# Kernel optimization log

Hardware: AMD Instinct MI355X
Metric: run time of the kernel (lower is better)

## Reference

```python
import jax, jax.numpy as jnp
import numpy as np

NUM_FRAMES = 8
HEAD_DIM = 32


def setup_inputs() -> dict:
    key = jax.random.key(0)
    k1, k2, k3, k4, k5 = jax.random.split(key, 5)
    dim = 384
    nh = dim // HEAD_DIM
    return {
        "x": jax.random.normal(k1, (16, dim, 16, 16), dtype=jnp.float32),
        "qk_w": jax.random.normal(k2, (2 * dim, dim), dtype=jnp.float32) * 0.02,
        "alpha": jax.random.normal(k3, (1, nh, 1, 1), dtype=jnp.float32),
        "beta": jax.random.normal(k4, (1, nh, 1, 1), dtype=jnp.float32),
        "gamma": jax.random.normal(k5, (1, nh, 1, 1), dtype=jnp.float32),
    }


def reference(x, qk_w, alpha, beta, gamma):
    B_T, C, H, W = x.shape
    B = B_T // NUM_FRAMES
    N = NUM_FRAMES * H * W
    nh = C // HEAD_DIM
    scale = HEAD_DIM ** -0.5

    # [B*T,C,H,W] -> [B,N,C] tokens (frames-major token order, matching torch)
    xt = x.reshape(B, NUM_FRAMES, C, H, W).transpose(0, 2, 1, 3, 4)  # B,C,T,H,W
    xt = xt.reshape(B, C, N).transpose(0, 2, 1)                      # B,N,C

    qk = (xt @ qk_w.T).reshape(B, N, 2, nh, HEAD_DIM)
    qk = qk.transpose(2, 0, 3, 1, 4)                                 # 2,B,nh,N,hd
    q, k = qk[0], qk[1]
    v = xt.reshape(B, N, nh, HEAD_DIM).transpose(0, 2, 1, 3)         # B,nh,N,hd

    attn = jax.nn.softmax(jnp.einsum('bhnd,bhmd->bhnm', q * scale, k), axis=-1)
    eye = jnp.eye(N, dtype=x.dtype)
    Cm = jnp.full((N, N), 1.0 / N, dtype=x.dtype)
    attn = alpha * eye + beta * attn - gamma * Cm                    # B,nh,N,N

    out = jnp.einsum('bhnm,bhmd->bhnd', attn, v)
    out = out.transpose(0, 2, 1, 3).reshape(B, N, C)                 # B,N,C
    out = out.transpose(0, 2, 1).reshape(B, C, NUM_FRAMES, H, W)
    out = out.transpose(0, 2, 1, 3, 4).reshape(B_T, C, H, W)
    return out
```

## Files before the change

kernel.cpp:

```cpp
#include <hip/hip_runtime.h>
#include <hip/hip_bf16.h>

typedef __attribute__((ext_vector_type(8))) short short8;
typedef __attribute__((ext_vector_type(4))) float f32x4;
typedef __attribute__((ext_vector_type(16))) float f32x16;
typedef __attribute__((ext_vector_type(4))) unsigned int uint4v;
typedef unsigned short ushort_t;
typedef unsigned int uint_t;

#define NFRAMES 8
#define HD 32
#define CDIM 384
#define NH 12
#define NTOK 2048
#define QKCOLS 768
#define TILEB 2048
#define QSCALE 0.2550541213313367f

static __device__ __forceinline__ ushort_t f2bf(float f) {
    __hip_bfloat16 h = __float2bfloat16(f);
    return *reinterpret_cast<ushort_t*>(&h);
}
static __device__ __forceinline__ uint_t packbf2(float lo, float hi) {
    return (uint_t)f2bf(lo) | ((uint_t)f2bf(hi) << 16);
}

__global__ __launch_bounds__(256) void pack_x_kernel(const float* __restrict__ x,
                                                     ushort_t* __restrict__ Xt,
                                                     ushort_t* __restrict__ VFG,
                                                     float* __restrict__ psum) {
    __shared__ float lds[32 * 256];
    __shared__ float red[8][32];
    int bt = blockIdx.x;
    int h = blockIdx.y;
    int tid = threadIdx.x;
    int c0 = h * 32;
    const float* src = x + ((long)bt * CDIM + c0) * 256;
#pragma unroll
    for (int i = 0; i < 32; ++i) lds[i * 256 + tid] = src[i * 256 + tid];
    __syncthreads();
    int b = bt >> 3, t = bt & 7;
    long n = (long)b * NTOK + t * 256 + tid;
    uint4* dst = reinterpret_cast<uint4*>(Xt + n * CDIM + c0);
#pragma unroll
    for (int k = 0; k < 4; ++k) {
        uint_t vv[4];
#pragma unroll
        for (int q = 0; q < 4; ++q)
            vv[q] = packbf2(lds[(k * 8 + q * 2) * 256 + tid], lds[(k * 8 + q * 2 + 1) * 256 + tid]);
        dst[k] = make_uint4(vv[0], vv[1], vv[2], vv[3]);
    }
    int bh = b * NH + h;
#pragma unroll
    for (int pass = 0; pass < 4; ++pass) {
        int kt = pass * 2 + (tid >> 7);
        int slot = tid & 127;
        int d = slot & 31, c2 = slot >> 5;
        const float* p0 = &lds[d * 256 + kt * 32 + c2 * 8];
        float4 a = *(const float4*)p0;
        float4 bb = *(const float4*)(p0 + 4);
        uint4 o = make_uint4(packbf2(a.x, a.y), packbf2(a.z, a.w),
                             packbf2(bb.x, bb.y), packbf2(bb.z, bb.w));
        *(uint4*)((char*)VFG + ((size_t)(bh * 64 + t * 8 + kt)) * TILEB + slot * 16) = o;
    }
    int ch = tid & 31, seg = tid >> 5;
    float s = 0.f;
#pragma unroll
    for (int j = 0; j < 32; ++j) s += lds[ch * 256 + seg * 32 + j];
    red[seg][ch] = s;
    __syncthreads();
    if (tid < 32) {
        float tot = 0.f;
#pragma unroll
        for (int i = 0; i < 8; ++i) tot += red[i][tid];
        psum[(bt * NH + h) * HD + tid] = tot;
    }
}

__global__ __launch_bounds__(256) void pack_w_kernel(const float* __restrict__ w,
                                                     ushort_t* __restrict__ Wb) {
    int idx = blockIdx.x * 256 + threadIdx.x;
    if (idx >= QKCOLS * CDIM) return;
    int j = idx / CDIM;
    float scale = (j < CDIM) ? QSCALE : 1.0f;
    Wb[idx] = f2bf(w[idx] * scale);
}

__global__ __launch_bounds__(256) void proj_kernel(const ushort_t* __restrict__ Xt,
                                                   const ushort_t* __restrict__ Wb,
                                                   ushort_t* __restrict__ QFG,
                                                   ushort_t* __restrict__ KFG) {
    __shared__ __align__(16) ushort_t tb[4][32][40];
    int tid = threadIdx.x;
    int lane = tid & 63;
    int w = tid >> 6;
    int wid = blockIdx.x * 4 + w;
    int mb = wid / 24, nb = wid % 24;
    int r16 = lane & 15, g = lane >> 4;
    const short8* A0 = reinterpret_cast<const short8*>(Xt + (mb * 32 + r16) * CDIM + g * 8);
    const short8* A1 = reinterpret_cast<const short8*>(Xt + (mb * 32 + 16 + r16) * CDIM + g * 8);
    const short8* B0 = reinterpret_cast<const short8*>(Wb + (nb * 32 + r16) * CDIM + g * 8);
    const short8* B1 = reinterpret_cast<const short8*>(Wb + (nb * 32 + 16 + r16) * CDIM + g * 8);
    f32x4 acc00{}, acc01{}, acc10{}, acc11{};
#pragma unroll
    for (int kk = 0; kk < 12; ++kk) {
        short8 a0 = A0[kk * 4];
        short8 a1 = A1[kk * 4];
        short8 b0 = B0[kk * 4];
        short8 b1 = B1[kk * 4];
        acc00 = __builtin_amdgcn_mfma_f32_16x16x32_bf16(a0, b0, acc00, 0, 0, 0);
        acc01 = __builtin_amdgcn_mfma_f32_16x16x32_bf16(a0, b1, acc01, 0, 0, 0);
        acc10 = __builtin_amdgcn_mfma_f32_16x16x32_bf16(a1, b0, acc10, 0, 0, 0);
        acc11 = __builtin_amdgcn_mfma_f32_16x16x32_bf16(a1, b1, acc11, 0, 0, 0);
    }
#pragma unroll
    for (int r = 0; r < 4; ++r) {
        int lr = g * 4 + r;
        tb[w][lr][r16] = f2bf(acc00[r]);
        tb[w][lr][r16 + 16] = f2bf(acc01[r]);
        tb[w][lr + 16][r16] = f2bf(acc10[r]);
        tb[w][lr + 16][r16 + 16] = f2bf(acc11[r]);
    }
    short8 f0 = *(const short8*)&tb[w][lane & 31][(lane >> 5) * 8];
    short8 f1 = *(const short8*)&tb[w][lane & 31][16 + (lane >> 5) * 8];
    int bsel = mb >> 6;
    int tile = mb & 63;
    int hh = (nb < 12) ? nb : nb - 12;
    ushort_t* dstbuf = (nb < 12) ? QFG : KFG;
    char* base = (char*)dstbuf + ((size_t)((bsel * NH + hh) * 64 + tile)) * TILEB;
    *(short8*)(base + lane * 16) = f0;
    *(short8*)(base + 1024 + lane * 16) = f1;
}

__global__ __launch_bounds__(256) void attn_kernel(
    const ushort_t* __restrict__ QFG, const ushort_t* __restrict__ KFG,
    const ushort_t* __restrict__ VFG, const float* __restrict__ x,
    const float* __restrict__ psum, const float* __restrict__ alpha,
    const float* __restrict__ beta, const float* __restrict__ gamma,
    float* __restrict__ out) {
    __shared__ float mrg[2240];

    int tid = threadIdx.x, lane = tid & 63, w = tid >> 6;
    int bid = blockIdx.x;
    int L = (bid & 7) * 96 + (bid >> 3);
    int rb = L & 31, bh = L >> 5;
    int h = bh % NH, b = bh / NH;
    int j31 = lane & 31, hi = lane >> 5;
    int qsub = w >> 1, kvpar = w & 1;
    int qb = rb * 64 + qsub * 32;

    const char* Qb = (const char*)QFG + ((size_t)(bh * 64 + rb * 2 + qsub)) * TILEB;
    short8 qf0 = *(const short8*)(Qb + lane * 16);
    short8 qf1 = *(const short8*)(Qb + 1024 + lane * 16);

    const char* Kbase = (const char*)KFG + (size_t)bh * 64 * TILEB + lane * 16;
    const char* Vbase = (const char*)VFG + (size_t)bh * 64 * TILEB + lane * 16;

    f32x16 acc = {};
    float lp = 0.f;

    short8 kA0, kA1, vA0, vA1, kB0, kB1, vB0, vB1;

#define LOADT(i, K0, K1, V0, V1)                                         \
    {                                                                    \
        size_t off = (size_t)(2 * (i) + kvpar) * TILEB;                  \
        K0 = *(const short8*)(Kbase + off);                              \
        K1 = *(const short8*)(Kbase + off + 1024);                       \
        V0 = *(const short8*)(Vbase + off);                              \
        V1 = *(const short8*)(Vbase + off + 1024);                       \
    }

#define COMPUTE(K0, K1, V0, V1)                                          \
    {                                                                    \
        f32x16 s = {};                                                   \
        s = __builtin_amdgcn_mfma_f32_32x32x16_bf16(K0, qf0, s, 0, 0, 0);\
        s = __builtin_amdgcn_mfma_f32_32x32x16_bf16(K1, qf1, s, 0, 0, 0);\
        float e[16];                                                     \
        _Pragma("unroll")                                                \
        for (int r = 0; r < 16; ++r) e[r] = __builtin_amdgcn_exp2f(s[r]);\
        lp += (((e[0] + e[1]) + (e[2] + e[3])) + ((e[4] + e[5]) + (e[6] + e[7]))) +  \
              (((e[8] + e[9]) + (e[10] + e[11])) + ((e[12] + e[13]) + (e[14] + e[15]))); \
        uint_t pk[8];                                                    \
        _Pragma("unroll")                                                \
        for (int j = 0; j < 8; ++j) pk[j] = packbf2(e[2 * j], e[2 * j + 1]); \
        _Pragma("unroll")                                                \
        for (int kh = 0; kh < 2; ++kh) {                                 \
            uint_t o0 = pk[kh * 4], o1 = pk[kh * 4 + 1];                 \
            uint_t o2 = pk[kh * 4 + 2], o3 = pk[kh * 4 + 3];             \
            uint_t s0_ = hi ? o0 : o2, s1_ = hi ? o1 : o3;               \
            uint_t g0 = __shfl_xor(s0_, 32), g1 = __shfl_xor(s1_, 32);   \
            uint4v uu;                                                   \
            uu[0] = hi ? g0 : o0;                                        \
            uu[1] = hi ? g1 : o1;                                        \
            uu[2] = hi ? o2 : g0;                                        \
            uu[3] = hi ? o3 : g1;                                        \
            short8 pa = __builtin_bit_cast(short8, uu);                  \
            acc = __builtin_amdgcn_mfma_f32_32x32x16_bf16(pa, (kh ? V1 : V0), acc, 0, 0, 0); \
        }                                                                \
    }

    LOADT(0, kA0, kA1, vA0, vA1);
#pragma unroll 2
    for (int i2 = 0; i2 < 16; ++i2) {
        int i = i2 * 2;
        if (i + 1 < 32) LOADT(i + 1, kB0, kB1, vB0, vB1);
        COMPUTE(kA0, kA1, vA0, vA1);
        if (i + 2 < 32) LOADT(i + 2, kA0, kA1, vA0, vA1);
        COMPUTE(kB0, kB1, vB0, vB1);
    }
#undef LOADT
#undef COMPUTE

    float* ab = mrg + qsub * 1088;
    if (kvpar) {
#pragma unroll
        for (int q = 0; q < 16; ++q) ab[lane * 17 + q] = acc[q];
        ab[lane * 17 + 16] = lp;
    }
    __syncthreads();
    float* Lb = mrg + 2176 + qsub * 32;
    if (!kvpar) {
#pragma unroll
        for (int q = 0; q < 16; ++q) acc[q] += ab[lane * 17 + q];
        float lsum = lp + ab[lane * 17 + 16];
        lsum += __shfl_xor(lsum, 32);
        if (!hi) Lb[j31] = lsum;
    }
    __syncthreads();
    if (!kvpar) {
        float alpha_h = alpha[h], beta_h = beta[h], gamma_h = gamma[h];
        int d = j31, c = h * HD + d;
        float sv = 0.f;
#pragma unroll
        for (int t = 0; t < NFRAMES; ++t) sv += psum[((b * NFRAMES + t) * NH + h) * HD + d];
        float gsv = gamma_h * sv * (1.0f / NTOK);
#pragma unroll
        for (int q = 0; q < 16; ++q) {
            int qrow = (q & 3) + 8 * (q >> 2) + 4 * hi;
            int n = qb + qrow;
            float linv = 1.0f / Lb[qrow];
            long xidx = ((long)(b * NFRAMES + (n >> 8)) * CDIM + c) * 256 + (n & 255);
            out[xidx] = beta_h * acc[q] * linv + alpha_h * x[xidx] - gsv;
        }
    }
}

extern "C" void kernel_launch(void* const* d_in, const int* in_sizes, int n_in,
                              void* d_out, int out_size, void* d_ws, size_t ws_size,
                              hipStream_t stream) {
    const float* x = (const float*)d_in[0];
    const float* qk_w = (const float*)d_in[1];
    const float* alpha = (const float*)d_in[2];
    const float* beta = (const float*)d_in[3];
    const float* gamma = (const float*)d_in[4];
    float* out = (float*)d_out;

    char* ws = (char*)d_ws;
    ushort_t* Xt = (ushort_t*)ws;
    ushort_t* Wb = (ushort_t*)(ws + 3145728);
    ushort_t* QFG = (ushort_t*)(ws + 3735552);
    ushort_t* KFG = (ushort_t*)(ws + 6881280);
    ushort_t* VFG = (ushort_t*)(ws + 10027008);
    float* psum = (float*)(ws + 13172736);

    hipLaunchKernelGGL(pack_x_kernel, dim3(16, 12), dim3(256), 0, stream, x, Xt, VFG, psum);
    hipLaunchKernelGGL(pack_w_kernel, dim3(1152), dim3(256), 0, stream, qk_w, Wb);
    hipLaunchKernelGGL(proj_kernel, dim3(768), dim3(256), 0, stream, Xt, Wb, QFG, KFG);
    hipLaunchKernelGGL(attn_kernel, dim3(768), dim3(256), 0, stream,
                       QFG, KFG, VFG, x, psum, alpha, beta, gamma, out);
}
```

Before: 61.53 us.

## Split attention KV four ways, fuse pack kernels, use 32x32 MFMA projection

The attention kernel now gives each block one 32-row query tile, with its four waves each covering a quarter of the keys. That doubles the grid and adds a three-way LDS merge and a wider partial-sum buffer. The two pack kernels are merged into one launch, and the weight pack is vectorised to 8 elements per thread. The projection uses one 32x32x16 MFMA chain per wave instead of four 16x16x32 tiles. In the softmax path, the bf16 conversion becomes a manual rounding with byte permute, the lane exchange uses permlane32_swap instead of shuffles, and the row-sum uses a float2 accumulator.

Measured after the change: 56.54 us. 1.09x faster.

```diff
diff --git a/kernel.cpp b/kernel.cpp
--- a/kernel.cpp
+++ b/kernel.cpp
@@ -3,6 +3,7 @@
 
 typedef __attribute__((ext_vector_type(8))) short short8;
 typedef __attribute__((ext_vector_type(4))) float f32x4;
+typedef __attribute__((ext_vector_type(2))) float f32x2;
 typedef __attribute__((ext_vector_type(16))) float f32x16;
 typedef __attribute__((ext_vector_type(4))) unsigned int uint4v;
 typedef unsigned short ushort_t;
@@ -25,15 +26,30 @@
     return (uint_t)f2bf(lo) | ((uint_t)f2bf(hi) << 16);
 }
 
-__global__ __launch_bounds__(256) void pack_x_kernel(const float* __restrict__ x,
-                                                     ushort_t* __restrict__ Xt,
-                                                     ushort_t* __restrict__ VFG,
-                                                     float* __restrict__ psum) {
+__global__ __launch_bounds__(256) void pack_kernel(const float* __restrict__ x,
+                                                   const float* __restrict__ qk_w,
+                                                   ushort_t* __restrict__ Xt,
+                                                   ushort_t* __restrict__ VFG,
+                                                   float* __restrict__ psum,
+                                                   ushort_t* __restrict__ Wb) {
+    int tid = threadIdx.x;
+    int bid = blockIdx.x;
+    if (bid >= 192) {
+        int vid = (bid - 192) * 256 + tid;
+        int j = vid / 48;
+        float scale = (j < CDIM) ? QSCALE : 1.0f;
+        const float* src = qk_w + vid * 8;
+        float4 a = *(const float4*)src;
+        float4 b = *(const float4*)(src + 4);
+        uint4 o = make_uint4(packbf2(a.x * scale, a.y * scale), packbf2(a.z * scale, a.w * scale),
+                             packbf2(b.x * scale, b.y * scale), packbf2(b.z * scale, b.w * scale));
+        *(uint4*)(Wb + vid * 8) = o;
+        return;
+    }
     __shared__ float lds[32 * 256];
     __shared__ float red[8][32];
-    int bt = blockIdx.x;
-    int h = blockIdx.y;
-    int tid = threadIdx.x;
+    int bt = bid & 15;
+    int h = bid >> 4;
     int c0 = h * 32;
     const float* src = x + ((long)bt * CDIM + c0) * 256;
 #pragma unroll
@@ -77,15 +93,6 @@
     }
 }
 
-__global__ __launch_bounds__(256) void pack_w_kernel(const float* __restrict__ w,
-                                                     ushort_t* __restrict__ Wb) {
-    int idx = blockIdx.x * 256 + threadIdx.x;
-    if (idx >= QKCOLS * CDIM) return;
-    int j = idx / CDIM;
-    float scale = (j < CDIM) ? QSCALE : 1.0f;
-    Wb[idx] = f2bf(w[idx] * scale);
-}
-
 __global__ __launch_bounds__(256) void proj_kernel(const ushort_t* __restrict__ Xt,
                                                    const ushort_t* __restrict__ Wb,
                                                    ushort_t* __restrict__ QFG,
@@ -96,33 +103,23 @@
     int w = tid >> 6;
     int wid = blockIdx.x * 4 + w;
     int mb = wid / 24, nb = wid % 24;
-    int r16 = lane & 15, g = lane >> 4;
-    const short8* A0 = reinterpret_cast<const short8*>(Xt + (mb * 32 + r16) * CDIM + g * 8);
-    const short8* A1 = reinterpret_cast<const short8*>(Xt + (mb * 32 + 16 + r16) * CDIM + g * 8);
-    const short8* B0 = reinterpret_cast<const short8*>(Wb + (nb * 32 + r16) * CDIM + g * 8);
-    const short8* B1 = reinterpret_cast<const short8*>(Wb + (nb * 32 + 16 + r16) * CDIM + g * 8);
-    f32x4 acc00{}, acc01{}, acc10{}, acc11{};
-#pragma unroll
-    for (int kk = 0; kk < 12; ++kk) {
-        short8 a0 = A0[kk * 4];
-        short8 a1 = A1[kk * 4];
-        short8 b0 = B0[kk * 4];
-        short8 b1 = B1[kk * 4];
-        acc00 = __builtin_amdgcn_mfma_f32_16x16x32_bf16(a0, b0, acc00, 0, 0, 0);
-        acc01 = __builtin_amdgcn_mfma_f32_16x16x32_bf16(a0, b1, acc01, 0, 0, 0);
-        acc10 = __builtin_amdgcn_mfma_f32_16x16x32_bf16(a1, b0, acc10, 0, 0, 0);
-        acc11 = __builtin_amdgcn_mfma_f32_16x16x32_bf16(a1, b1, acc11, 0, 0, 0);
-    }
-#pragma unroll
-    for (int r = 0; r < 4; ++r) {
-        int lr = g * 4 + r;
-        tb[w][lr][r16] = f2bf(acc00[r]);
-        tb[w][lr][r16 + 16] = f2bf(acc01[r]);
-        tb[w][lr + 16][r16] = f2bf(acc10[r]);
-        tb[w][lr + 16][r16 + 16] = f2bf(acc11[r]);
-    }
-    short8 f0 = *(const short8*)&tb[w][lane & 31][(lane >> 5) * 8];
-    short8 f1 = *(const short8*)&tb[w][lane & 31][16 + (lane >> 5) * 8];
+    int j31 = lane & 31, hi = lane >> 5;
+    const char* Arow = (const char*)(Xt + (mb * 32 + j31) * CDIM + hi * 8);
+    const char* Brow = (const char*)(Wb + (nb * 32 + j31) * CDIM + hi * 8);
+    f32x16 acc = {};
+#pragma unroll
+    for (int k16 = 0; k16 < 24; ++k16) {
+        short8 a = *(const short8*)(Arow + k16 * 32);
+        short8 bb = *(const short8*)(Brow + k16 * 32);
+        acc = __builtin_amdgcn_mfma_f32_32x32x16_bf16(a, bb, acc, 0, 0, 0);
+    }
+#pragma unroll
+    for (int q = 0; q < 16; ++q) {
+        int row = (q & 3) + 8 * (q >> 2) + 4 * hi;
+        tb[w][row][j31] = f2bf(acc[q]);
+    }
+    short8 f0 = *(const short8*)&tb[w][j31][hi * 8];
+    short8 f1 = *(const short8*)&tb[w][j31][16 + hi * 8];
     int bsel = mb >> 6;
     int tile = mb & 63;
     int hh = (nb < 12) ? nb : nb - 12;
@@ -138,96 +135,100 @@
     const float* __restrict__ psum, const float* __restrict__ alpha,
     const float* __restrict__ beta, const float* __restrict__ gamma,
     float* __restrict__ out) {
-    __shared__ float mrg[2240];
+    __shared__ float mrg[3 * 1088 + 32];
 
     int tid = threadIdx.x, lane = tid & 63, w = tid >> 6;
     int bid = blockIdx.x;
-    int L = (bid & 7) * 96 + (bid >> 3);
-    int rb = L & 31, bh = L >> 5;
+    int L = (bid & 7) * 192 + (bid >> 3);
+    int rb = L & 63, bh = L >> 6;
     int h = bh % NH, b = bh / NH;
     int j31 = lane & 31, hi = lane >> 5;
-    int qsub = w >> 1, kvpar = w & 1;
-    int qb = rb * 64 + qsub * 32;
-
-    const char* Qb = (const char*)QFG + ((size_t)(bh * 64 + rb * 2 + qsub)) * TILEB;
+    int qb = rb * 32;
+
+    const char* Qb = (const char*)QFG + ((size_t)(bh * 64 + rb)) * TILEB;
     short8 qf0 = *(const short8*)(Qb + lane * 16);
     short8 qf1 = *(const short8*)(Qb + 1024 + lane * 16);
 
-    const char* Kbase = (const char*)KFG + (size_t)bh * 64 * TILEB + lane * 16;
-    const char* Vbase = (const char*)VFG + (size_t)bh * 64 * TILEB + lane * 16;
+    const char* Kbase = (const char*)KFG + ((size_t)(bh * 64 + w * 16)) * TILEB + lane * 16;
+    const char* Vbase = (const char*)VFG + ((size_t)(bh * 64 + w * 16)) * TILEB + lane * 16;
 
     f32x16 acc = {};
-    float lp = 0.f;
+    f32x2 lp2 = {};
 
     short8 kA0, kA1, vA0, vA1, kB0, kB1, vB0, vB1;
 
-#define LOADT(i, K0, K1, V0, V1)                                         \
-    {                                                                    \
-        size_t off = (size_t)(2 * (i) + kvpar) * TILEB;                  \
-        K0 = *(const short8*)(Kbase + off);                              \
-        K1 = *(const short8*)(Kbase + off + 1024);                       \
-        V0 = *(const short8*)(Vbase + off);                              \
-        V1 = *(const short8*)(Vbase + off + 1024);                       \
-    }
-
-#define COMPUTE(K0, K1, V0, V1)                                          \
-    {                                                                    \
-        f32x16 s = {};                                                   \
-        s = __builtin_amdgcn_mfma_f32_32x32x16_bf16(K0, qf0, s, 0, 0, 0);\
-        s = __builtin_amdgcn_mfma_f32_32x32x16_bf16(K1, qf1, s, 0, 0, 0);\
-        float e[16];                                                     \
-        _Pragma("unroll")                                                \
-        for (int r = 0; r < 16; ++r) e[r] = __builtin_amdgcn_exp2f(s[r]);\
-        lp += (((e[0] + e[1]) + (e[2] + e[3])) + ((e[4] + e[5]) + (e[6] + e[7]))) +  \
-              (((e[8] + e[9]) + (e[10] + e[11])) + ((e[12] + e[13]) + (e[14] + e[15]))); \
-        uint_t pk[8];                                                    \
-        _Pragma("unroll")                                                \
-        for (int j = 0; j < 8; ++j) pk[j] = packbf2(e[2 * j], e[2 * j + 1]); \
-        _Pragma("unroll")                                                \
-        for (int kh = 0; kh < 2; ++kh) {                                 \
-            uint_t o0 = pk[kh * 4], o1 = pk[kh * 4 + 1];                 \
-            uint_t o2 = pk[kh * 4 + 2], o3 = pk[kh * 4 + 3];             \
-            uint_t s0_ = hi ? o0 : o2, s1_ = hi ? o1 : o3;               \
-            uint_t g0 = __shfl_xor(s0_, 32), g1 = __shfl_xor(s1_, 32);   \
-            uint4v uu;                                                   \
-            uu[0] = hi ? g0 : o0;                                        \
-            uu[1] = hi ? g1 : o1;                                        \
-            uu[2] = hi ? o2 : g0;                                        \
-            uu[3] = hi ? o3 : g1;                                        \
-            short8 pa = __builtin_bit_cast(short8, uu);                  \
+#define LOADT(i, K0, K1, V0, V1)                              \
+    {                                                         \
+        size_t off = (size_t)(i)*TILEB;                       \
+        K0 = *(const short8*)(Kbase + off);                   \
+        K1 = *(const short8*)(Kbase + off + 1024);            \
+        V0 = *(const short8*)(Vbase + off);                   \
+        V1 = *(const short8*)(Vbase + off + 1024);            \
+    }
+
+#define COMPUTE(K0, K1, V0, V1)                                                    \
+    {                                                                              \
+        f32x16 s = {};                                                             \
+        s = __builtin_amdgcn_mfma_f32_32x32x16_bf16(K0, qf0, s, 0, 0, 0);          \
+        s = __builtin_amdgcn_mfma_f32_32x32x16_bf16(K1, qf1, s, 0, 0, 0);          \
+        uint_t pk[8];                                                              \
+        _Pragma("unroll")                                                          \
+        for (int j = 0; j < 8; ++j) {                                              \
+            float e0 = __builtin_amdgcn_exp2f(s[2 * j]);                           \
+            float e1 = __builtin_amdgcn_exp2f(s[2 * j + 1]);                       \
+            uint_t u0 = __builtin_bit_cast(uint_t, e0) + 0x8000u;                  \
+            uint_t u1 = __builtin_bit_cast(uint_t, e1) + 0x8000u;                  \
+            pk[j] = __builtin_amdgcn_perm(u1, u0, 0x07060302u);                    \
+            f32x2 ee;                                                              \
+            ee[0] = e0;                                                            \
+            ee[1] = e1;                                                            \
+            lp2 += ee;                                                             \
+        }                                                                          \
+        _Pragma("unroll")                                                          \
+        for (int kh = 0; kh < 2; ++kh) {                                           \
+            uint_t o0 = pk[kh * 4], o1 = pk[kh * 4 + 1];                           \
+            uint_t o2 = pk[kh * 4 + 2], o3 = pk[kh * 4 + 3];                       \
+            auto r02 = __builtin_amdgcn_permlane32_swap(o2, o0, false, false);     \
+            auto r13 = __builtin_amdgcn_permlane32_swap(o3, o1, false, false);     \
+            uint4v uu;                                                             \
+            uu[0] = r02[1];                                  \
+            uu[1] = r13[1];                                  \
+            uu[2] = r02[0];                                  \
+            uu[3] = r13[0];                                  \
+            short8 pa = __builtin_bit_cast(short8, uu);                            \
             acc = __builtin_amdgcn_mfma_f32_32x32x16_bf16(pa, (kh ? V1 : V0), acc, 0, 0, 0); \
-        }                                                                \
+        }                                                                          \
     }
 
     LOADT(0, kA0, kA1, vA0, vA1);
-#pragma unroll 2
-    for (int i2 = 0; i2 < 16; ++i2) {
+#pragma unroll
+    for (int i2 = 0; i2 < 8; ++i2) {
         int i = i2 * 2;
-        if (i + 1 < 32) LOADT(i + 1, kB0, kB1, vB0, vB1);
+        if (i + 1 < 16) LOADT(i + 1, kB0, kB1, vB0, vB1);
         COMPUTE(kA0, kA1, vA0, vA1);
-        if (i + 2 < 32) LOADT(i + 2, kA0, kA1, vA0, vA1);
+        if (i + 2 < 16) LOADT(i + 2, kA0, kA1, vA0, vA1);
         COMPUTE(kB0, kB1, vB0, vB1);
     }
 #undef LOADT
 #undef COMPUTE
 
-    float* ab = mrg + qsub * 1088;
-    if (kvpar) {
+    float lp = lp2[0] + lp2[1];
+
+    if (w) {
+        float* ab = mrg + (w - 1) * 1088;
 #pragma unroll
         for (int q = 0; q < 16; ++q) ab[lane * 17 + q] = acc[q];
         ab[lane * 17 + 16] = lp;
     }
     __syncthreads();
-    float* Lb = mrg + 2176 + qsub * 32;
-    if (!kvpar) {
-#pragma unroll
-        for (int q = 0; q < 16; ++q) acc[q] += ab[lane * 17 + q];
-        float lsum = lp + ab[lane * 17 + 16];
+    if (w == 0) {
+#pragma unroll
+        for (int q = 0; q < 16; ++q)
+            acc[q] += mrg[lane * 17 + q] + mrg[1088 + lane * 17 + q] + mrg[2176 + lane * 17 + q];
+        float lsum = lp + mrg[lane * 17 + 16] + mrg[1088 + lane * 17 + 16] + mrg[2176 + lane * 17 + 16];
         lsum += __shfl_xor(lsum, 32);
+        float* Lb = mrg + 3 * 1088;
         if (!hi) Lb[j31] = lsum;
-    }
-    __syncthreads();
-    if (!kvpar) {
         float alpha_h = alpha[h], beta_h = beta[h], gamma_h = gamma[h];
         int d = j31, c = h * HD + d;
         float sv = 0.f;
@@ -263,9 +264,8 @@
     ushort_t* VFG = (ushort_t*)(ws + 10027008);
     float* psum = (float*)(ws + 13172736);
 
-    hipLaunchKernelGGL(pack_x_kernel, dim3(16, 12), dim3(256), 0, stream, x, Xt, VFG, psum);
-    hipLaunchKernelGGL(pack_w_kernel, dim3(1152), dim3(256), 0, stream, qk_w, Wb);
+    hipLaunchKernelGGL(pack_kernel, dim3(336), dim3(256), 0, stream, x, qk_w, Xt, VFG, psum, Wb);
     hipLaunchKernelGGL(proj_kernel, dim3(768), dim3(256), 0, stream, Xt, Wb, QFG, KFG);
-    hipLaunchKernelGGL(attn_kernel, dim3(768), dim3(256), 0, stream,
+    hipLaunchKernelGGL(attn_kernel, dim3(1536), dim3(256), 0, stream,
                        QFG, KFG, VFG, x, psum, alpha, beta, gamma, out);
 }
```
